# Optimization experiments

Measured on AMD Instinct MI355X. Metric: run time of the kernel, lower is better.

## Reference

```python
import jax, jax.numpy as jnp
import numpy as np

TEMPERATURE = 8.0   # sqrt(d_k), d_k = 64
TOP_K = 5           # SparseAttention default top_k in mimicry/RIMs
EPS = 1e-7          # matches torch 10e-8


def _sparsify(attn_rows):
    """Per-row top-k sparsification: keep mass above the k-th largest value,
    clamp at zero, renormalize. attn_rows: [N, L]."""
    topk_vals = jax.lax.top_k(attn_rows, TOP_K)[0]          # [N, K]
    delta = topk_vals[:, -1:] + EPS                          # k-th largest per row
    w = jnp.maximum(attn_rows - delta, 0.0)                  # clamp(min=0)
    return w / (jnp.sum(w, axis=1, keepdims=True) + EPS)


def setup_inputs() -> dict:
    key = jax.random.key(0)
    kq, kk, kv = jax.random.split(key, 3)
    B, L, D = 4, 4096, 64
    q = jax.random.normal(kq, (B, L, D), dtype=jnp.float32)
    k = jax.random.normal(kk, (B, L, D), dtype=jnp.float32)
    v = jax.random.normal(kv, (B, L, D), dtype=jnp.float32)
    return {"q": q, "k": k, "v": v}


def reference(q, k, v):
    # attn = softmax(q k^T / temperature); dropout is identity in eval mode
    attn = jnp.einsum('bqd,bkd->bqk', q / TEMPERATURE, k)   # [B, Lq, Lk]
    attn = jax.nn.softmax(attn, axis=-1)
    B, Lq, Lk = attn.shape
    attn = _sparsify(attn.reshape(B * Lq, Lk)).reshape(B, Lq, Lk)
    out = jnp.einsum('bqk,bkd->bqd', attn, v)               # [B, Lq, Dv]
    return out, attn
```

## Files before the change

kernel.cpp:

```cpp
#include <hip/hip_runtime.h>
#include <math.h>

#define NB 4
#define L 4096
#define D 64
#define QPB 64
#define TCOLS 128
#define NT (L / TCOLS)
#define KCH (TCOLS + 1)
#define QCH (QPB + 1)

typedef __attribute__((ext_vector_type(8))) short short8;
typedef __attribute__((ext_vector_type(4))) float floatx4;

static __device__ inline ushort2 f2bf2(float x) {
    unsigned int u = __builtin_bit_cast(unsigned int, x);
    unsigned int uh = u + (0x7FFFu + ((u >> 16) & 1u));
    unsigned short h = (unsigned short)(uh >> 16);
    float hf = __builtin_bit_cast(float, (unsigned int)h << 16);
    float r = x - hf;
    unsigned int v = __builtin_bit_cast(unsigned int, r);
    unsigned short l = (unsigned short)((v + (0x7FFFu + ((v >> 16) & 1u))) >> 16);
    ushort2 p; p.x = h; p.y = l; return p;
}

__global__ __launch_bounds__(256, 1)
void sparse_attn_kernel(const float* __restrict__ qg,
                        const float* __restrict__ kg,
                        const float* __restrict__ vg,
                        float* __restrict__ outg) {
    __shared__ unsigned short skth[2][8 * KCH * 8];
    __shared__ unsigned short sktl[2][8 * KCH * 8];
    __shared__ unsigned short sqh[8 * QCH * 8];
    __shared__ unsigned short sql[8 * QCH * 8];

    const int tid  = threadIdx.x;
    const int lane = tid & 63;
    const int wid  = tid >> 6;
    const int c16  = lane & 15;
    const int quad = lane >> 4;

    const int sblk  = (blockIdx.x & 7) * 32 + (blockIdx.x >> 3);
    const int qbase = sblk * QPB;
    const int b     = qbase >> 12;
    const float* kb = kg + (size_t)b * L * D;
    const float* vb = vg + (size_t)b * L * D;
    float* attng = outg + (size_t)NB * L * D;
    float4* zrow = (float4*)(attng + (size_t)qbase * L);

#pragma unroll
    for (int i = 0; i < 4; ++i) {
        int f   = tid + i * 256;
        int row = f >> 4, f4 = f & 15;
        float4 qv = *(const float4*)(qg + (size_t)(qbase + row) * D + f4 * 4);
        ushort2 p0 = f2bf2(qv.x), p1 = f2bf2(qv.y), p2 = f2bf2(qv.z), p3 = f2bf2(qv.w);
        int base = (((f4 >> 1) * QCH) + row) * 8 + (f4 & 1) * 4;
        ushort4 ph; ph.x = p0.x; ph.y = p1.x; ph.z = p2.x; ph.w = p3.x;
        ushort4 pl; pl.x = p0.y; pl.y = p1.y; pl.z = p2.y; pl.w = p3.y;
        *(ushort4*)&sqh[base] = ph;
        *(ushort4*)&sql[base] = pl;
    }

    float4 r8[8];
#pragma unroll
    for (int i = 0; i < 8; ++i)
        r8[i] = *(const float4*)(kb + (tid + i * 256) * 4);
#pragma unroll
    for (int i = 0; i < 8; ++i) {
        int f = tid + i * 256;
        int col = f >> 4, f4 = f & 15;
        ushort2 p0 = f2bf2(r8[i].x), p1 = f2bf2(r8[i].y), p2 = f2bf2(r8[i].z), p3 = f2bf2(r8[i].w);
        int base = (((f4 >> 1) * KCH) + col) * 8 + (f4 & 1) * 4;
        ushort4 ph; ph.x = p0.x; ph.y = p1.x; ph.z = p2.x; ph.w = p3.x;
        ushort4 pl; pl.x = p0.y; pl.y = p1.y; pl.z = p2.y; pl.w = p3.y;
        *(ushort4*)&skth[0][base] = ph;
        *(ushort4*)&sktl[0][base] = pl;
    }
#pragma unroll
    for (int i = 0; i < 8; ++i)
        r8[i] = *(const float4*)(kb + (size_t)1 * TCOLS * D + (tid + i * 256) * 4);

    __syncthreads();

    const short8 a0h = *(const short8*)&sqh[((quad)     * QCH + wid * 16 + c16) * 8];
    const short8 a1h = *(const short8*)&sqh[((4 + quad) * QCH + wid * 16 + c16) * 8];
    const short8 a0l = *(const short8*)&sql[((quad)     * QCH + wid * 16 + c16) * 8];
    const short8 a1l = *(const short8*)&sql[((4 + quad) * QCH + wid * 16 + c16) * 8];

    float Z[4] = {0.f, 0.f, 0.f, 0.f};
    float tv[4][5];
    int   tc[4][5];
#pragma unroll
    for (int r = 0; r < 4; ++r)
#pragma unroll
        for (int i = 0; i < 5; ++i) { tv[r][i] = -INFINITY; tc[r][i] = -1; }

    for (int g = 0; g < NT; ++g) {
        const unsigned short* kbh = skth[g & 1];
        const unsigned short* kbl = sktl[g & 1];

#pragma unroll
        for (int cg = 0; cg < 8; ++cg) {
            short8 b0h = *(const short8*)&kbh[((quad)     * KCH + cg * 16 + c16) * 8];
            short8 b1h = *(const short8*)&kbh[((4 + quad) * KCH + cg * 16 + c16) * 8];
            short8 b0l = *(const short8*)&kbl[((quad)     * KCH + cg * 16 + c16) * 8];
            short8 b1l = *(const short8*)&kbl[((4 + quad) * KCH + cg * 16 + c16) * 8];
            floatx4 acc = {0.f, 0.f, 0.f, 0.f};
            acc = __builtin_amdgcn_mfma_f32_16x16x32_bf16(a0h, b0h, acc, 0, 0, 0);
            acc = __builtin_amdgcn_mfma_f32_16x16x32_bf16(a1h, b1h, acc, 0, 0, 0);
            acc = __builtin_amdgcn_mfma_f32_16x16x32_bf16(a0l, b0h, acc, 0, 0, 0);
            acc = __builtin_amdgcn_mfma_f32_16x16x32_bf16(a1l, b1h, acc, 0, 0, 0);
            acc = __builtin_amdgcn_mfma_f32_16x16x32_bf16(a0h, b0l, acc, 0, 0, 0);
            acc = __builtin_amdgcn_mfma_f32_16x16x32_bf16(a1h, b1l, acc, 0, 0, 0);
            int col = g * TCOLS + cg * 16 + c16;
#pragma unroll
            for (int r = 0; r < 4; ++r) {
                float s = acc[r] * 0.125f;
                Z[r] += __expf(s);
                bool q0 = s > tv[r][0];
                bool q1 = s > tv[r][1];
                bool q2 = s > tv[r][2];
                bool q3 = s > tv[r][3];
                bool q4 = s > tv[r][4];
                tv[r][4] = q4 ? (q3 ? tv[r][3] : s)   : tv[r][4];
                tc[r][4] = q4 ? (q3 ? tc[r][3] : col) : tc[r][4];
                tv[r][3] = q3 ? (q2 ? tv[r][2] : s)   : tv[r][3];
                tc[r][3] = q3 ? (q2 ? tc[r][2] : col) : tc[r][3];
                tv[r][2] = q2 ? (q1 ? tv[r][1] : s)   : tv[r][2];
                tc[r][2] = q2 ? (q1 ? tc[r][1] : col) : tc[r][2];
                tv[r][1] = q1 ? (q0 ? tv[r][0] : s)   : tv[r][1];
                tc[r][1] = q1 ? (q0 ? tc[r][0] : col) : tc[r][1];
                tv[r][0] = q0 ? s   : tv[r][0];
                tc[r][0] = q0 ? col : tc[r][0];
            }
        }

        float4 zv = make_float4(0.f, 0.f, 0.f, 0.f);
#pragma unroll
        for (int j = 0; j < 8; ++j)
            zrow[(size_t)(g * 8 + j) * 256 + tid] = zv;

        if (g + 1 < NT) {
#pragma unroll
            for (int i = 0; i < 8; ++i) {
                int f = tid + i * 256;
                int col = f >> 4, f4 = f & 15;
                ushort2 p0 = f2bf2(r8[i].x), p1 = f2bf2(r8[i].y),
                        p2 = f2bf2(r8[i].z), p3 = f2bf2(r8[i].w);
                int base = (((f4 >> 1) * KCH) + col) * 8 + (f4 & 1) * 4;
                ushort4 ph; ph.x = p0.x; ph.y = p1.x; ph.z = p2.x; ph.w = p3.x;
                ushort4 pl; pl.x = p0.y; pl.y = p1.y; pl.z = p2.y; pl.w = p3.y;
                *(ushort4*)&skth[(g + 1) & 1][base] = ph;
                *(ushort4*)&sktl[(g + 1) & 1][base] = pl;
            }
            if (g + 2 < NT) {
#pragma unroll
                for (int i = 0; i < 8; ++i)
                    r8[i] = *(const float4*)(kb + (size_t)(g + 2) * TCOLS * D + (tid + i * 256) * 4);
            }
        }
        __syncthreads();
    }

#pragma unroll
    for (int r = 0; r < 4; ++r) {
        float z = Z[r];
        z += __shfl_xor(z, 1, 64);
        z += __shfl_xor(z, 2, 64);
        z += __shfl_xor(z, 4, 64);
        z += __shfl_xor(z, 8, 64);

        float gv[5]; int gc[5];
#pragma unroll
        for (int k5 = 0; k5 < 5; ++k5) {
            float cv = tv[r][0]; int cc = tc[r][0];
#pragma unroll
            for (int m = 8; m >= 1; m >>= 1) {
                float ov = __shfl_xor(cv, m, 64);
                int   oc = __shfl_xor(cc, m, 64);
                if (ov > cv || (ov == cv && oc < cc)) { cv = ov; cc = oc; }
            }
            gv[k5] = cv; gc[k5] = cc;
            if (tc[r][0] == cc) {
                tv[r][0] = tv[r][1]; tc[r][0] = tc[r][1];
                tv[r][1] = tv[r][2]; tc[r][1] = tc[r][2];
                tv[r][2] = tv[r][3]; tc[r][2] = tc[r][3];
                tv[r][3] = tv[r][4]; tc[r][3] = tc[r][4];
                tv[r][4] = -INFINITY; tc[r][4] = -1;
            }
        }

        float invz = 1.0f / z;
        float e0 = __expf(gv[0]) * invz;
        float e1 = __expf(gv[1]) * invz;
        float e2 = __expf(gv[2]) * invz;
        float e3 = __expf(gv[3]) * invz;
        float e4 = __expf(gv[4]) * invz;
        float delta = e4 + 1e-7f;
        float w0 = fmaxf(e0 - delta, 0.f);
        float w1 = fmaxf(e1 - delta, 0.f);
        float w2 = fmaxf(e2 - delta, 0.f);
        float w3 = fmaxf(e3 - delta, 0.f);
        float inv = 1.0f / (w0 + w1 + w2 + w3 + 1e-7f);
        w0 *= inv; w1 *= inv; w2 *= inv; w3 *= inv;

        const int rowabs = qbase + wid * 16 + quad * 4 + r;

        const float4 v0 = *(const float4*)(vb + (size_t)gc[0] * D + c16 * 4);
        const float4 v1 = *(const float4*)(vb + (size_t)gc[1] * D + c16 * 4);
        const float4 v2 = *(const float4*)(vb + (size_t)gc[2] * D + c16 * 4);
        const float4 v3 = *(const float4*)(vb + (size_t)gc[3] * D + c16 * 4);
        float4 o;
        o.x = w0 * v0.x + w1 * v1.x + w2 * v2.x + w3 * v3.x;
        o.y = w0 * v0.y + w1 * v1.y + w2 * v2.y + w3 * v3.y;
        o.z = w0 * v0.z + w1 * v1.z + w2 * v2.z + w3 * v3.z;
        o.w = w0 * v0.w + w1 * v1.w + w2 * v2.w + w3 * v3.w;
        *(float4*)(outg + (size_t)rowabs * D + c16 * 4) = o;

        if (c16 < 4) {
            float wv = c16 == 0 ? w0 : c16 == 1 ? w1 : c16 == 2 ? w2 : w3;
            int   cs = c16 == 0 ? gc[0] : c16 == 1 ? gc[1] : c16 == 2 ? gc[2] : gc[3];
            attng[(size_t)rowabs * L + cs] = wv;
        }
    }
}

extern "C" void kernel_launch(void* const* d_in, const int* in_sizes, int n_in,
                              void* d_out, int out_size, void* d_ws, size_t ws_size,
                              hipStream_t stream) {
    const float* q = (const float*)d_in[0];
    const float* k = (const float*)d_in[1];
    const float* v = (const float*)d_in[2];
    float* out = (float*)d_out;

    dim3 grid(NB * L / QPB);
    sparse_attn_kernel<<<grid, 256, 0, stream>>>(q, k, v, out);
}
```

Measured before the change: 343.9 us.

## Pre-convert Q/K to split-bf16 in workspace, DMA K tiles to LDS, split columns across waves

Adds a separate pre-pass kernel that converts Q and K to hi/lo bf16 pairs once, writing K in the tile-major LDS layout to a workspace. The attention kernel then streams each K tile straight into LDS with global_load_lds DMA instead of converting per block. It also doubles the block to 512 threads, so two wave groups each handle half of every tile's columns; their per-row top-5 and exp sums are merged through shared memory at the end. This removes redundant per-block K conversion and register staging, at the cost of an extra launch, workspace traffic, and a final cross-wave merge step.

```diff
diff --git a/kernel.cpp b/kernel.cpp
--- a/kernel.cpp
+++ b/kernel.cpp
@@ -7,11 +7,10 @@
 #define QPB 64
 #define TCOLS 128
 #define NT (L / TCOLS)
-#define KCH (TCOLS + 1)
-#define QCH (QPB + 1)
 
 typedef __attribute__((ext_vector_type(8))) short short8;
 typedef __attribute__((ext_vector_type(4))) float floatx4;
+typedef unsigned int u32;
 
 static __device__ inline ushort2 f2bf2(float x) {
     unsigned int u = __builtin_bit_cast(unsigned int, x);
@@ -24,68 +23,84 @@
     ushort2 p; p.x = h; p.y = l; return p;
 }
 
-__global__ __launch_bounds__(256, 1)
-void sparse_attn_kernel(const float* __restrict__ qg,
-                        const float* __restrict__ kg,
+static __device__ inline void dma16(const unsigned short* g, unsigned short* l) {
+    __builtin_amdgcn_global_load_lds(
+        (const __attribute__((address_space(1))) u32*)g,
+        (__attribute__((address_space(3))) u32*)l, 16, 0, 0);
+}
+
+#define WS_QL 1048576
+#define WS_KW 2097152
+
+__global__ __launch_bounds__(256)
+void convert_kernel(const float* __restrict__ qg, const float* __restrict__ kg,
+                    unsigned short* __restrict__ ws) {
+    unsigned int i = blockIdx.x * 256 + threadIdx.x;
+    if (i < 262144) {
+        float4 qv = ((const float4*)qg)[i];
+        ushort2 p0 = f2bf2(qv.x), p1 = f2bf2(qv.y), p2 = f2bf2(qv.z), p3 = f2bf2(qv.w);
+        ushort4 h; h.x = p0.x; h.y = p1.x; h.z = p2.x; h.w = p3.x;
+        ushort4 l; l.x = p0.y; l.y = p1.y; l.z = p2.y; l.w = p3.y;
+        *(ushort4*)&ws[i * 4] = h;
+        *(ushort4*)&ws[WS_QL + i * 4] = l;
+    } else {
+        unsigned int j = i - 262144;
+        float4 kv = ((const float4*)kg)[j];
+        ushort2 p0 = f2bf2(kv.x), p1 = f2bf2(kv.y), p2 = f2bf2(kv.z), p3 = f2bf2(kv.w);
+        ushort4 h; h.x = p0.x; h.y = p1.x; h.z = p2.x; h.w = p3.x;
+        ushort4 l; l.x = p0.y; l.y = p1.y; l.z = p2.y; l.w = p3.y;
+        unsigned int bcol = j >> 4;
+        unsigned int f4   = j & 15;
+        unsigned int tile = bcol >> 7;
+        unsigned int tcol = bcol & 127;
+        unsigned int cq   = f4 >> 1, half = f4 & 1;
+        unsigned int base = tile * 16384 + (cq * 128 + tcol) * 8 + half * 4;
+        *(ushort4*)&ws[WS_KW + base] = h;
+        *(ushort4*)&ws[WS_KW + base + 8192] = l;
+    }
+}
+
+__global__ __launch_bounds__(512, 2)
+void sparse_attn_kernel(const unsigned short* __restrict__ ws,
                         const float* __restrict__ vg,
                         float* __restrict__ outg) {
-    __shared__ unsigned short skth[2][8 * KCH * 8];
-    __shared__ unsigned short sktl[2][8 * KCH * 8];
-    __shared__ unsigned short sqh[8 * QCH * 8];
-    __shared__ unsigned short sql[8 * QCH * 8];
+    __shared__ unsigned short skt[2][16384];
+    __shared__ float smv[QPB][5];
+    __shared__ int   smc[QPB][5];
+    __shared__ float smz[QPB];
 
     const int tid  = threadIdx.x;
     const int lane = tid & 63;
-    const int wid  = tid >> 6;
+    const int w    = tid >> 6;
+    const int rg   = w & 3;
+    const int ch   = w >> 2;
     const int c16  = lane & 15;
     const int quad = lane >> 4;
 
     const int sblk  = (blockIdx.x & 7) * 32 + (blockIdx.x >> 3);
     const int qbase = sblk * QPB;
     const int b     = qbase >> 12;
-    const float* kb = kg + (size_t)b * L * D;
+
+    const unsigned short* qh = ws;
+    const unsigned short* ql = ws + WS_QL;
+    const unsigned short* kw = ws + WS_KW + (size_t)b * NT * 16384;
+
     const float* vb = vg + (size_t)b * L * D;
     float* attng = outg + (size_t)NB * L * D;
     float4* zrow = (float4*)(attng + (size_t)qbase * L);
 
-#pragma unroll
-    for (int i = 0; i < 4; ++i) {
-        int f   = tid + i * 256;
-        int row = f >> 4, f4 = f & 15;
-        float4 qv = *(const float4*)(qg + (size_t)(qbase + row) * D + f4 * 4);
-        ushort2 p0 = f2bf2(qv.x), p1 = f2bf2(qv.y), p2 = f2bf2(qv.z), p3 = f2bf2(qv.w);
-        int base = (((f4 >> 1) * QCH) + row) * 8 + (f4 & 1) * 4;
-        ushort4 ph; ph.x = p0.x; ph.y = p1.x; ph.z = p2.x; ph.w = p3.x;
-        ushort4 pl; pl.x = p0.y; pl.y = p1.y; pl.z = p2.y; pl.w = p3.y;
-        *(ushort4*)&sqh[base] = ph;
-        *(ushort4*)&sql[base] = pl;
-    }
-
-    float4 r8[8];
-#pragma unroll
-    for (int i = 0; i < 8; ++i)
-        r8[i] = *(const float4*)(kb + (tid + i * 256) * 4);
-#pragma unroll
-    for (int i = 0; i < 8; ++i) {
-        int f = tid + i * 256;
-        int col = f >> 4, f4 = f & 15;
-        ushort2 p0 = f2bf2(r8[i].x), p1 = f2bf2(r8[i].y), p2 = f2bf2(r8[i].z), p3 = f2bf2(r8[i].w);
-        int base = (((f4 >> 1) * KCH) + col) * 8 + (f4 & 1) * 4;
-        ushort4 ph; ph.x = p0.x; ph.y = p1.x; ph.z = p2.x; ph.w = p3.x;
-        ushort4 pl; pl.x = p0.y; pl.y = p1.y; pl.z = p2.y; pl.w = p3.y;
-        *(ushort4*)&skth[0][base] = ph;
-        *(ushort4*)&sktl[0][base] = pl;
-    }
-#pragma unroll
-    for (int i = 0; i < 8; ++i)
-        r8[i] = *(const float4*)(kb + (size_t)1 * TCOLS * D + (tid + i * 256) * 4);
-
+    const int qrow = qbase + rg * 16 + c16;
+    const short8 a0h = *(const short8*)&qh[(size_t)qrow * 64 + quad * 8];
+    const short8 a1h = *(const short8*)&qh[(size_t)qrow * 64 + 32 + quad * 8];
+    const short8 a0l = *(const short8*)&ql[(size_t)qrow * 64 + quad * 8];
+    const short8 a1l = *(const short8*)&ql[(size_t)qrow * 64 + 32 + quad * 8];
+
+#pragma unroll
+    for (int jj = 0; jj < 4; ++jj) {
+        int idx = w * 4 + jj;
+        dma16(kw + idx * 512 + lane * 8, &skt[0][idx * 512]);
+    }
     __syncthreads();
-
-    const short8 a0h = *(const short8*)&sqh[((quad)     * QCH + wid * 16 + c16) * 8];
-    const short8 a1h = *(const short8*)&sqh[((4 + quad) * QCH + wid * 16 + c16) * 8];
-    const short8 a0l = *(const short8*)&sql[((quad)     * QCH + wid * 16 + c16) * 8];
-    const short8 a1l = *(const short8*)&sql[((4 + quad) * QCH + wid * 16 + c16) * 8];
 
     float Z[4] = {0.f, 0.f, 0.f, 0.f};
     float tv[4][5];
@@ -96,15 +111,26 @@
         for (int i = 0; i < 5; ++i) { tv[r][i] = -INFINITY; tc[r][i] = -1; }
 
     for (int g = 0; g < NT; ++g) {
-        const unsigned short* kbh = skth[g & 1];
-        const unsigned short* kbl = sktl[g & 1];
-
-#pragma unroll
-        for (int cg = 0; cg < 8; ++cg) {
-            short8 b0h = *(const short8*)&kbh[((quad)     * KCH + cg * 16 + c16) * 8];
-            short8 b1h = *(const short8*)&kbh[((4 + quad) * KCH + cg * 16 + c16) * 8];
-            short8 b0l = *(const short8*)&kbl[((quad)     * KCH + cg * 16 + c16) * 8];
-            short8 b1l = *(const short8*)&kbl[((4 + quad) * KCH + cg * 16 + c16) * 8];
+        if (g + 1 < NT) {
+#pragma unroll
+            for (int jj = 0; jj < 4; ++jj) {
+                int idx = w * 4 + jj;
+                dma16(kw + (g + 1) * 16384 + idx * 512 + lane * 8,
+                      &skt[(g + 1) & 1][idx * 512]);
+            }
+        }
+
+        const unsigned short* kbh = skt[g & 1];
+        const unsigned short* kbl = skt[g & 1] + 8192;
+
+#pragma unroll
+        for (int j = 0; j < 4; ++j) {
+            const int cg = ch * 4 + j;
+            const int cb = cg * 16 + c16;
+            short8 b0h = *(const short8*)&kbh[((quad)     * 128 + cb) * 8];
+            short8 b1h = *(const short8*)&kbh[((4 + quad) * 128 + cb) * 8];
+            short8 b0l = *(const short8*)&kbl[((quad)     * 128 + cb) * 8];
+            short8 b1l = *(const short8*)&kbl[((4 + quad) * 128 + cb) * 8];
             floatx4 acc = {0.f, 0.f, 0.f, 0.f};
             acc = __builtin_amdgcn_mfma_f32_16x16x32_bf16(a0h, b0h, acc, 0, 0, 0);
             acc = __builtin_amdgcn_mfma_f32_16x16x32_bf16(a1h, b1h, acc, 0, 0, 0);
@@ -112,7 +138,7 @@
             acc = __builtin_amdgcn_mfma_f32_16x16x32_bf16(a1l, b1h, acc, 0, 0, 0);
             acc = __builtin_amdgcn_mfma_f32_16x16x32_bf16(a0h, b0l, acc, 0, 0, 0);
             acc = __builtin_amdgcn_mfma_f32_16x16x32_bf16(a1h, b1l, acc, 0, 0, 0);
-            int col = g * TCOLS + cg * 16 + c16;
+            const int col = g * TCOLS + cb;
 #pragma unroll
             for (int r = 0; r < 4; ++r) {
                 float s = acc[r] * 0.125f;
@@ -137,31 +163,13 @@
 
         float4 zv = make_float4(0.f, 0.f, 0.f, 0.f);
 #pragma unroll
-        for (int j = 0; j < 8; ++j)
-            zrow[(size_t)(g * 8 + j) * 256 + tid] = zv;
-
-        if (g + 1 < NT) {
-#pragma unroll
-            for (int i = 0; i < 8; ++i) {
-                int f = tid + i * 256;
-                int col = f >> 4, f4 = f & 15;
-                ushort2 p0 = f2bf2(r8[i].x), p1 = f2bf2(r8[i].y),
-                        p2 = f2bf2(r8[i].z), p3 = f2bf2(r8[i].w);
-                int base = (((f4 >> 1) * KCH) + col) * 8 + (f4 & 1) * 4;
-                ushort4 ph; ph.x = p0.x; ph.y = p1.x; ph.z = p2.x; ph.w = p3.x;
-                ushort4 pl; pl.x = p0.y; pl.y = p1.y; pl.z = p2.y; pl.w = p3.y;
-                *(ushort4*)&skth[(g + 1) & 1][base] = ph;
-                *(ushort4*)&sktl[(g + 1) & 1][base] = pl;
-            }
-            if (g + 2 < NT) {
-#pragma unroll
-                for (int i = 0; i < 8; ++i)
-                    r8[i] = *(const float4*)(kb + (size_t)(g + 2) * TCOLS * D + (tid + i * 256) * 4);
-            }
-        }
+        for (int jj = 0; jj < 4; ++jj)
+            zrow[(size_t)g * 2048 + jj * 512 + tid] = zv;
+
         __syncthreads();
     }
 
+    float gv[4][5]; int gc[4][5]; float zz[4];
 #pragma unroll
     for (int r = 0; r < 4; ++r) {
         float z = Z[r];
@@ -169,8 +177,8 @@
         z += __shfl_xor(z, 2, 64);
         z += __shfl_xor(z, 4, 64);
         z += __shfl_xor(z, 8, 64);
-
-        float gv[5]; int gc[5];
+        zz[r] = z;
+        const int rowl = rg * 16 + quad * 4 + r;
 #pragma unroll
         for (int k5 = 0; k5 < 5; ++k5) {
             float cv = tv[r][0]; int cc = tc[r][0];
@@ -180,7 +188,8 @@
                 int   oc = __shfl_xor(cc, m, 64);
                 if (ov > cv || (ov == cv && oc < cc)) { cv = ov; cc = oc; }
             }
-            gv[k5] = cv; gc[k5] = cc;
+            gv[r][k5] = cv; gc[r][k5] = cc;
+            if (ch == 1 && c16 == k5) { smv[rowl][k5] = cv; smc[rowl][k5] = cc; }
             if (tc[r][0] == cc) {
                 tv[r][0] = tv[r][1]; tc[r][0] = tc[r][1];
                 tv[r][1] = tv[r][2]; tc[r][1] = tc[r][2];
@@ -189,38 +198,69 @@
                 tv[r][4] = -INFINITY; tc[r][4] = -1;
             }
         }
-
-        float invz = 1.0f / z;
-        float e0 = __expf(gv[0]) * invz;
-        float e1 = __expf(gv[1]) * invz;
-        float e2 = __expf(gv[2]) * invz;
-        float e3 = __expf(gv[3]) * invz;
-        float e4 = __expf(gv[4]) * invz;
-        float delta = e4 + 1e-7f;
-        float w0 = fmaxf(e0 - delta, 0.f);
-        float w1 = fmaxf(e1 - delta, 0.f);
-        float w2 = fmaxf(e2 - delta, 0.f);
-        float w3 = fmaxf(e3 - delta, 0.f);
-        float inv = 1.0f / (w0 + w1 + w2 + w3 + 1e-7f);
-        w0 *= inv; w1 *= inv; w2 *= inv; w3 *= inv;
-
-        const int rowabs = qbase + wid * 16 + quad * 4 + r;
-
-        const float4 v0 = *(const float4*)(vb + (size_t)gc[0] * D + c16 * 4);
-        const float4 v1 = *(const float4*)(vb + (size_t)gc[1] * D + c16 * 4);
-        const float4 v2 = *(const float4*)(vb + (size_t)gc[2] * D + c16 * 4);
-        const float4 v3 = *(const float4*)(vb + (size_t)gc[3] * D + c16 * 4);
-        float4 o;
-        o.x = w0 * v0.x + w1 * v1.x + w2 * v2.x + w3 * v3.x;
-        o.y = w0 * v0.y + w1 * v1.y + w2 * v2.y + w3 * v3.y;
-        o.z = w0 * v0.z + w1 * v1.z + w2 * v2.z + w3 * v3.z;
-        o.w = w0 * v0.w + w1 * v1.w + w2 * v2.w + w3 * v3.w;
-        *(float4*)(outg + (size_t)rowabs * D + c16 * 4) = o;
-
-        if (c16 < 4) {
-            float wv = c16 == 0 ? w0 : c16 == 1 ? w1 : c16 == 2 ? w2 : w3;
-            int   cs = c16 == 0 ? gc[0] : c16 == 1 ? gc[1] : c16 == 2 ? gc[2] : gc[3];
-            attng[(size_t)rowabs * L + cs] = wv;
+        if (ch == 1 && c16 == 5) smz[rowl] = z;
+    }
+    __syncthreads();
+
+    if (ch == 0) {
+#pragma unroll
+        for (int r = 0; r < 4; ++r) {
+            const int rowl = rg * 16 + quad * 4 + r;
+            float z = zz[r] + smz[rowl];
+#pragma unroll
+            for (int f = 0; f < 5; ++f) {
+                float fv = smv[rowl][f];
+                int   fc = smc[rowl][f];
+                bool q0 = fv > gv[r][0];
+                bool q1 = fv > gv[r][1];
+                bool q2 = fv > gv[r][2];
+                bool q3 = fv > gv[r][3];
+                bool q4 = fv > gv[r][4];
+                gv[r][4] = q4 ? (q3 ? gv[r][3] : fv) : gv[r][4];
+                gc[r][4] = q4 ? (q3 ? gc[r][3] : fc) : gc[r][4];
+                gv[r][3] = q3 ? (q2 ? gv[r][2] : fv) : gv[r][3];
+                gc[r][3] = q3 ? (q2 ? gc[r][2] : fc) : gc[r][3];
+                gv[r][2] = q2 ? (q1 ? gv[r][1] : fv) : gv[r][2];
+                gc[r][2] = q2 ? (q1 ? gc[r][1] : fc) : gc[r][2];
+                gv[r][1] = q1 ? (q0 ? gv[r][0] : fv) : gv[r][1];
+                gc[r][1] = q1 ? (q0 ? gc[r][0] : fc) : gc[r][1];
+                gv[r][0] = q0 ? fv : gv[r][0];
+                gc[r][0] = q0 ? fc : gc[r][0];
+            }
+
+            float invz = 1.0f / z;
+            float e0 = __expf(gv[r][0]) * invz;
+            float e1 = __expf(gv[r][1]) * invz;
+            float e2 = __expf(gv[r][2]) * invz;
+            float e3 = __expf(gv[r][3]) * invz;
+            float e4 = __expf(gv[r][4]) * invz;
+            float delta = e4 + 1e-7f;
+            float w0 = fmaxf(e0 - delta, 0.f);
+            float w1 = fmaxf(e1 - delta, 0.f);
+            float w2 = fmaxf(e2 - delta, 0.f);
+            float w3 = fmaxf(e3 - delta, 0.f);
+            float inv = 1.0f / (w0 + w1 + w2 + w3 + 1e-7f);
+            w0 *= inv; w1 *= inv; w2 *= inv; w3 *= inv;
+
+            const int rowabs = qbase + rowl;
+
+            const float4 v0 = *(const float4*)(vb + (size_t)gc[r][0] * D + c16 * 4);
+            const float4 v1 = *(const float4*)(vb + (size_t)gc[r][1] * D + c16 * 4);
+            const float4 v2 = *(const float4*)(vb + (size_t)gc[r][2] * D + c16 * 4);
+            const float4 v3 = *(const float4*)(vb + (size_t)gc[r][3] * D + c16 * 4);
+            float4 o;
+            o.x = w0 * v0.x + w1 * v1.x + w2 * v2.x + w3 * v3.x;
+            o.y = w0 * v0.y + w1 * v1.y + w2 * v2.y + w3 * v3.y;
+            o.z = w0 * v0.z + w1 * v1.z + w2 * v2.z + w3 * v3.z;
+            o.w = w0 * v0.w + w1 * v1.w + w2 * v2.w + w3 * v3.w;
+            *(float4*)(outg + (size_t)rowabs * D + c16 * 4) = o;
+
+            if (c16 < 4) {
+                float wv = c16 == 0 ? w0 : c16 == 1 ? w1 : c16 == 2 ? w2 : w3;
+                int   cs = c16 == 0 ? gc[r][0] : c16 == 1 ? gc[r][1]
+                         : c16 == 2 ? gc[r][2] : gc[r][3];
+                attng[(size_t)rowabs * L + cs] = wv;
+            }
         }
     }
 }
@@ -232,7 +272,10 @@
     const float* k = (const float*)d_in[1];
     const float* v = (const float*)d_in[2];
     float* out = (float*)d_out;
+    unsigned short* ws = (unsigned short*)d_ws;
+
+    convert_kernel<<<2048, 256, 0, stream>>>(q, k, ws);
 
     dim3 grid(NB * L / QPB);
-    sparse_attn_kernel<<<grid, 256, 0, stream>>>(q, k, v, out);
-}
+    sparse_attn_kernel<<<grid, 512, 0, stream>>>(ws, v, out);
+}
```

After: 346.5 us. About the same (+0.7%).
